# Kernel tuning notes

Measured on AMD Instinct MI355X. Metric: run time of the kernel, lower is better.

Reference implementation:

```python
import jax, jax.numpy as jnp
import numpy as np
from jax.ops import segment_sum

N_NODES = 50000
N_EDGES = 800000
D_IN, D_HID, D_OUT = 128, 128, 64


def setup_inputs() -> dict:
    key = jax.random.key(0)
    ks = jax.random.split(key, 7)
    return {
        "src": jax.random.randint(ks[0], (N_EDGES,), 0, N_NODES, dtype=jnp.int32),
        "dst": jax.random.randint(ks[1], (N_EDGES,), 0, N_NODES, dtype=jnp.int32),
        "x": jax.random.normal(ks[2], (N_NODES, D_IN), dtype=jnp.float32),
        "W1": jax.random.normal(ks[3], (D_IN, D_HID), dtype=jnp.float32) * (1.0 / np.sqrt(D_IN)),
        "b1": jnp.zeros((D_HID,), dtype=jnp.float32),
        "W2": jax.random.normal(ks[4], (D_HID, D_OUT), dtype=jnp.float32) * (1.0 / np.sqrt(D_HID)),
        "b2": jnp.zeros((D_OUT,), dtype=jnp.float32),
    }


def _gcn_layer(src, dst, x, W, b, inv_sqrt_out, inv_sqrt_in):
    # DGL GraphConv, norm='both': h = D_in^{-1/2} A D_out^{-1/2} (x W) + b
    h = (x * inv_sqrt_out[:, None]) @ W          # transform first (in >= out)
    msg = h[src]                                  # gather source messages [E, d]
    agg = segment_sum(msg, dst, num_segments=x.shape[0])
    return agg * inv_sqrt_in[:, None] + b


def reference(src, dst, x, W1, b1, W2, b2):
    n = x.shape[0]
    ones = jnp.ones((src.shape[0],), dtype=x.dtype)
    deg_out = jnp.clip(segment_sum(ones, src, num_segments=n), 1.0)
    deg_in = jnp.clip(segment_sum(ones, dst, num_segments=n), 1.0)
    inv_sqrt_out = jax.lax.rsqrt(deg_out)
    inv_sqrt_in = jax.lax.rsqrt(deg_in)
    h = _gcn_layer(src, dst, x, W1, b1, inv_sqrt_out, inv_sqrt_in)
    h = jax.nn.relu(h)
    h = _gcn_layer(src, dst, h, W2, b2, inv_sqrt_out, inv_sqrt_in)
    return h
```

## Files before the change

kernel.cpp:

```cpp
#include <hip/hip_runtime.h>
#include <hip/hip_fp16.h>

#define D_IN  128
#define D_HID 128
#define D_OUT 64
#define NBMAX 512
#define CHUNK 2048
#define BM 128
#define BK 32
#define FCACHE 3072

__global__ void k_zero(int* __restrict__ cntD, int* __restrict__ cntS, int NB) {
    const int t = threadIdx.x;
    if (t < NB) { cntD[t] = 0; cntS[t] = 0; }
}

__launch_bounds__(256)
__global__ void k_bucket(const int* __restrict__ src, const int* __restrict__ dst,
                         int E, int NB, int cap,
                         int* __restrict__ cntD, int* __restrict__ cntS,
                         unsigned int* __restrict__ storeD, unsigned char* __restrict__ storeS) {
    __shared__ int lcD[NBMAX], lcS[NBMAX];
    __shared__ int lbD[NBMAX], lbS[NBMAX];
    const int t = threadIdx.x;
    const int e0 = blockIdx.x * CHUNK;
    const int e1 = min(e0 + CHUNK, E);

    for (int i = t; i < NB; i += 256) { lcD[i] = 0; lcS[i] = 0; }
    __syncthreads();
    for (int i = e0 + t; i < e1; i += 256) {
        atomicAdd(&lcD[dst[i] >> 7], 1);
        atomicAdd(&lcS[src[i] >> 7], 1);
    }
    __syncthreads();
    for (int i = t; i < NB; i += 256) {
        lbD[i] = lcD[i] ? atomicAdd(&cntD[i], lcD[i]) : 0;
        lbS[i] = lcS[i] ? atomicAdd(&cntS[i], lcS[i]) : 0;
        lcD[i] = 0; lcS[i] = 0;
    }
    __syncthreads();
    for (int i = e0 + t; i < e1; i += 256) {
        const int s = src[i], d = dst[i];
        const int bd = d >> 7;
        const int pd = lbD[bd] + atomicAdd(&lcD[bd], 1);
        storeD[(long long)bd * cap + pd] = (unsigned int)s | ((unsigned int)(d & 127) << 16);
        const int bs = s >> 7;
        const int ps = lbS[bs] + atomicAdd(&lcS[bs], 1);
        storeS[(long long)bs * cap + ps] = (unsigned char)(s & 127);
    }
}

__launch_bounds__(256)
__global__ void k_fin(const unsigned int* __restrict__ storeD, const unsigned char* __restrict__ storeS,
                      const int* __restrict__ cntD, const int* __restrict__ cntS,
                      int cap, int N, int NB, int E,
                      int* __restrict__ rowptr, float* __restrict__ inv_in,
                      float* __restrict__ inv_out, unsigned short* __restrict__ csr_src) {
    __shared__ int fh[128];
    __shared__ int sc[128];
    __shared__ int cur[128];
    __shared__ int red[256];
    __shared__ unsigned int ecache[FCACHE];
    const int b = blockIdx.x, t = threadIdx.x;
    const long long sb = (long long)b * cap;

    int partial = 0;
    for (int i = t; i < b; i += 256) partial += cntD[i];
    red[t] = partial;
    __syncthreads();
    for (int off = 128; off > 0; off >>= 1) {
        if (t < off) red[t] += red[t + off];
        __syncthreads();
    }
    const int base = red[0];

    const int cnt = cntD[b];
    const bool cached = (cnt <= FCACHE);
    if (cached) {
        for (int i = t; i < cnt; i += 256) ecache[i] = storeD[sb + i];
    }

    if (t < 128) fh[t] = 0;
    __syncthreads();
    for (int i = t; i < cnt; i += 256) {
        const unsigned int e = cached ? ecache[i] : storeD[sb + i];
        atomicAdd(&fh[e >> 16], 1);
    }
    __syncthreads();
    if (t < 128) sc[t] = fh[t];
    __syncthreads();
    int inc = (t < 128) ? sc[t] : 0;
    for (int off = 1; off < 128; off <<= 1) {
        int o = (t >= off && t < 128) ? sc[t - off] : 0;
        __syncthreads();
        if (t < 128) { inc += o; sc[t] = inc; }
        __syncthreads();
    }
    if (t < 128) {
        const int excl = inc - fh[t];
        cur[t] = excl;
        const int node = (b << 7) + t;
        if (node < N) {
            rowptr[node] = base + excl;
            inv_in[node] = rsqrtf((float)max(fh[t], 1));
        }
    }
    if (b == NB - 1 && t == 128) rowptr[N] = E;
    __syncthreads();
    for (int i = t; i < cnt; i += 256) {
        const unsigned int e = cached ? ecache[i] : storeD[sb + i];
        const int pos = atomicAdd(&cur[e >> 16], 1);
        csr_src[base + pos] = (unsigned short)(e & 0xFFFFu);
    }

    __syncthreads();
    if (t < 128) fh[t] = 0;
    __syncthreads();
    const int cnts = cntS[b];
    for (int i = t; i < cnts; i += 256) atomicAdd(&fh[storeS[sb + i]], 1);
    __syncthreads();
    if (t < 128) {
        const int node = (b << 7) + t;
        if (node < N) inv_out[node] = rsqrtf((float)max(fh[t], 1));
    }
}

template<int LDN>
__launch_bounds__(256)
__global__ void k_gemm3(const float* __restrict__ X, const float* __restrict__ W,
                        const float* __restrict__ scale, __half* __restrict__ Y, int N) {
    __shared__ float As[BK][BM + 4];
    __shared__ float Bs[BK][64];

    const int t  = threadIdx.x;
    const int tx = t & 15;
    const int ty = t >> 4;
    const int row0 = blockIdx.x * BM;
    const int col0 = blockIdx.y * 64;

    const int xr = t >> 3;
    const int xc = (t & 7) * 4;

    float acc[8][4];
#pragma unroll
    for (int m = 0; m < 8; ++m)
#pragma unroll
        for (int n = 0; n < 4; ++n) acc[m][n] = 0.0f;

    for (int kk = 0; kk < D_IN; kk += BK) {
        __syncthreads();
#pragma unroll
        for (int p = 0; p < 4; ++p) {
            const int r  = p * 32 + xr;
            const int gr = row0 + r;
            float4 v = make_float4(0.f, 0.f, 0.f, 0.f);
            if (gr < N) {
                v = *(const float4*)(X + (long long)gr * D_IN + kk + xc);
                if (scale) { const float s = scale[gr]; v.x *= s; v.y *= s; v.z *= s; v.w *= s; }
            }
            As[xc + 0][r] = v.x;
            As[xc + 1][r] = v.y;
            As[xc + 2][r] = v.z;
            As[xc + 3][r] = v.w;
        }
#pragma unroll
        for (int p = 0; p < 2; ++p) {
            const int flat = p * 256 + t;
            const int kr = flat >> 4;
            const int jc = (flat & 15) * 4;
            *(float4*)&Bs[kr][jc] = *(const float4*)(W + (long long)(kk + kr) * LDN + col0 + jc);
        }
        __syncthreads();

#pragma unroll
        for (int k = 0; k < BK; ++k) {
            const float4 a0 = *(const float4*)&As[k][ty * 8];
            const float4 a1 = *(const float4*)&As[k][ty * 8 + 4];
            const float4 b0 = *(const float4*)&Bs[k][tx * 4];
            const float am[8] = {a0.x, a0.y, a0.z, a0.w, a1.x, a1.y, a1.z, a1.w};
            const float bn[4] = {b0.x, b0.y, b0.z, b0.w};
#pragma unroll
            for (int m = 0; m < 8; ++m)
#pragma unroll
                for (int n = 0; n < 4; ++n)
                    acc[m][n] += am[m] * bn[n];
        }
    }

#pragma unroll
    for (int m = 0; m < 8; ++m) {
        const int gr = row0 + ty * 8 + m;
        if (gr < N) {
            __half2 h0 = __float22half2_rn(make_float2(acc[m][0], acc[m][1]));
            __half2 h1 = __float22half2_rn(make_float2(acc[m][2], acc[m][3]));
            uint2 pk;
            pk.x = *(unsigned int*)&h0;
            pk.y = *(unsigned int*)&h1;
            *(uint2*)(Y + (long long)gr * LDN + col0 + tx * 4) = pk;
        }
    }
}

template<int D, bool RELU>
__launch_bounds__(256)
__global__ void k_gather(const int* __restrict__ rowptr, const unsigned short* __restrict__ csr_src,
                         const __half* __restrict__ Y, const float* __restrict__ inv_in,
                         const float* __restrict__ inv_out, const float* __restrict__ b,
                         float* __restrict__ out, int N) {
    const int wid  = (int)((blockIdx.x * 256u + threadIdx.x) >> 6);
    const int lane = threadIdx.x & 63;
    if (wid >= N) return;

    const int start = rowptr[wid];
    const int end   = rowptr[wid + 1];

    constexpr int LPE = D / 8;
    constexpr int EPW = 64 / LPE;
    const int grp  = lane / LPE;
    const int colh = (lane % LPE) * 8;

    float a[8];
#pragma unroll
    for (int u = 0; u < 8; ++u) a[u] = 0.0f;

    auto accum = [&](uint4 raw) {
        const __half2* h = (const __half2*)&raw;
#pragma unroll
        for (int u = 0; u < 4; ++u) {
            const float2 f = __half22float2(h[u]);
            a[2 * u]     += f.x;
            a[2 * u + 1] += f.y;
        }
    };

    for (int k = start; k < end; k += 64) {
        const int idx = k + lane;
        const int sv  = (idx < end) ? (int)csr_src[idx] : 0;
        const int cnt = min(64, end - k);
        int j = 0;
        for (; j + 4 * EPW <= cnt; j += 4 * EPW) {
            const int s0 = __shfl(sv, j + grp);
            const int s1 = __shfl(sv, j + EPW + grp);
            const int s2 = __shfl(sv, j + 2 * EPW + grp);
            const int s3 = __shfl(sv, j + 3 * EPW + grp);
            const uint4 r0 = *(const uint4*)(Y + (long long)s0 * D + colh);
            const uint4 r1 = *(const uint4*)(Y + (long long)s1 * D + colh);
            const uint4 r2 = *(const uint4*)(Y + (long long)s2 * D + colh);
            const uint4 r3 = *(const uint4*)(Y + (long long)s3 * D + colh);
            accum(r0); accum(r1); accum(r2); accum(r3);
        }
        for (; j < cnt; j += EPW) {
            const int jj = j + grp;
            const int s  = __shfl(sv, jj);
            if (jj < cnt) {
                const uint4 r = *(const uint4*)(Y + (long long)s * D + colh);
                accum(r);
            }
        }
    }

#pragma unroll
    for (int u = 0; u < 8; ++u) a[u] += __shfl_down(a[u], 32);
#pragma unroll
    for (int u = 0; u < 8; ++u) a[u] += __shfl_down(a[u], 16);
    if (EPW == 8) {
#pragma unroll
        for (int u = 0; u < 8; ++u) a[u] += __shfl_down(a[u], 8);
    }

    if (lane < LPE) {
        const float ii = inv_in[wid];
        const float io = RELU ? inv_out[wid] : 0.0f;
        const float4 b0 = *(const float4*)(b + colh);
        const float4 b1 = *(const float4*)(b + colh + 4);
        float r[8];
        r[0] = a[0] * ii + b0.x; r[1] = a[1] * ii + b0.y;
        r[2] = a[2] * ii + b0.z; r[3] = a[3] * ii + b0.w;
        r[4] = a[4] * ii + b1.x; r[5] = a[5] * ii + b1.y;
        r[6] = a[6] * ii + b1.z; r[7] = a[7] * ii + b1.w;
        if (RELU) {
#pragma unroll
            for (int u = 0; u < 8; ++u) r[u] = fmaxf(r[u], 0.0f) * io;
        }
        float* o = out + (long long)wid * D + colh;
        *(float4*)(o)     = make_float4(r[0], r[1], r[2], r[3]);
        *(float4*)(o + 4) = make_float4(r[4], r[5], r[6], r[7]);
    }
}

extern "C" void kernel_launch(void* const* d_in, const int* in_sizes, int n_in,
                              void* d_out, int out_size, void* d_ws, size_t ws_size,
                              hipStream_t stream) {
    const int*   src = (const int*)d_in[0];
    const int*   dst = (const int*)d_in[1];
    const float* x   = (const float*)d_in[2];
    const float* W1  = (const float*)d_in[3];
    const float* b1  = (const float*)d_in[4];
    const float* W2  = (const float*)d_in[5];
    const float* b2  = (const float*)d_in[6];
    float* out = (float*)d_out;

    const int E  = in_sizes[0];
    const int N  = in_sizes[2] / D_IN;
    const int NB = (N + 127) >> 7;
    const int mean = E / NB;
    const int cap  = mean + mean / 4 + 128;

    char* ws = (char*)d_ws;
    size_t off = 0;
    auto alloc = [&](size_t bytes) -> void* {
        void* p = ws + off;
        off += (bytes + 255) & ~(size_t)255;
        return p;
    };
    float*          inv_out = (float*)alloc((size_t)N * 4);
    float*          inv_in  = (float*)alloc((size_t)N * 4);
    int*            rowptr  = (int*)alloc((size_t)(N + 1) * 4);
    int*            cntD    = (int*)alloc((size_t)NB * 4);
    int*            cntS    = (int*)alloc((size_t)NB * 4);
    unsigned int*   storeD  = (unsigned int*)alloc((size_t)NB * cap * 4);
    unsigned char*  storeS  = (unsigned char*)alloc((size_t)NB * cap);
    unsigned short* csr_src = (unsigned short*)alloc((size_t)E * 2);
    __half*         Y1      = (__half*)alloc((size_t)N * D_HID * 2);
    float*          H       = (float*)alloc((size_t)N * D_HID * 4);
    __half*         Y2      = (__half*)alloc((size_t)N * D_OUT * 2);
    (void)ws_size; (void)n_in; (void)out_size;

    k_zero<<<1, 512, 0, stream>>>(cntD, cntS, NB);
    k_bucket<<<(E + CHUNK - 1) / CHUNK, 256, 0, stream>>>(src, dst, E, NB, cap, cntD, cntS, storeD, storeS);
    k_fin<<<NB, 256, 0, stream>>>(storeD, storeS, cntD, cntS, cap, N, NB, E,
                                  rowptr, inv_in, inv_out, csr_src);

    {
        dim3 g((N + BM - 1) / BM, D_HID / 64);
        k_gemm3<D_HID><<<g, 256, 0, stream>>>(x, W1, inv_out, Y1, N);
    }
    k_gather<D_HID, true><<<(N + 3) / 4, 256, 0, stream>>>(rowptr, csr_src, Y1, inv_in, inv_out, b1, H, N);

    {
        dim3 g((N + BM - 1) / BM, D_OUT / 64);
        k_gemm3<D_OUT><<<g, 256, 0, stream>>>(H, W2, nullptr, Y2, N);
    }
    k_gather<D_OUT, false><<<(N + 3) / 4, 256, 0, stream>>>(rowptr, csr_src, Y2, inv_in, nullptr, b2, out, N);
}
```

Before: 144.0 us.

## Use split-bf16 MFMA GEMMs and store hidden activations in fp16

Replaces the FP32 SIMT tiled GEMM with a matrix-core kernel. Each FP32 operand is split into high and low bf16 parts, and three MFMA products approximate FP32 accuracy. The hidden activation H written by the first gather is now fp16 instead of fp32, which halves its write and read traffic. This costs extra conversion work when staging into LDS, a smaller 32-row tile with W reloaded per block, and some precision loss in H.

```diff
diff --git a/kernel.cpp b/kernel.cpp
--- a/kernel.cpp
+++ b/kernel.cpp
@@ -6,9 +6,15 @@
 #define D_OUT 64
 #define NBMAX 512
 #define CHUNK 2048
-#define BM 128
-#define BK 32
 #define FCACHE 3072
+
+typedef __attribute__((ext_vector_type(8))) short bf16x8;
+typedef __attribute__((ext_vector_type(4))) float f32x4;
+
+__device__ __forceinline__ unsigned short f2bf_rne(float f) {
+    unsigned int u = __float_as_uint(f);
+    return (unsigned short)((u + 0x7FFFu + ((u >> 16) & 1u)) >> 16);
+}
 
 __global__ void k_zero(int* __restrict__ cntD, int* __restrict__ cntS, int NB) {
     const int t = threadIdx.x;
@@ -125,88 +131,132 @@
     }
 }
 
-template<int LDN>
+template<int LDN, typename TA>
 __launch_bounds__(256)
-__global__ void k_gemm3(const float* __restrict__ X, const float* __restrict__ W,
-                        const float* __restrict__ scale, __half* __restrict__ Y, int N) {
-    __shared__ float As[BK][BM + 4];
-    __shared__ float Bs[BK][64];
-
-    const int t  = threadIdx.x;
-    const int tx = t & 15;
-    const int ty = t >> 4;
-    const int row0 = blockIdx.x * BM;
+__global__ void k_gemm_mfma(const TA* __restrict__ X, const float* __restrict__ W,
+                            const float* __restrict__ scale, __half* __restrict__ Y, int N) {
+    __shared__ short Ah[32][136], Al[32][136];
+    __shared__ short Bh[64][136], Bl[64][136];
+
+    const int t = threadIdx.x;
+    const int row0 = blockIdx.x * 32;
     const int col0 = blockIdx.y * 64;
 
-    const int xr = t >> 3;
-    const int xc = (t & 7) * 4;
-
-    float acc[8][4];
-#pragma unroll
-    for (int m = 0; m < 8; ++m)
-#pragma unroll
-        for (int n = 0; n < 4; ++n) acc[m][n] = 0.0f;
-
-    for (int kk = 0; kk < D_IN; kk += BK) {
-        __syncthreads();
+    if constexpr (sizeof(TA) == 4) {
 #pragma unroll
         for (int p = 0; p < 4; ++p) {
-            const int r  = p * 32 + xr;
-            const int gr = row0 + r;
+            const int idx = p * 256 + t;
+            const int r   = idx >> 5;
+            const int c4  = (idx & 31) << 2;
+            const int gr  = row0 + r;
             float4 v = make_float4(0.f, 0.f, 0.f, 0.f);
             if (gr < N) {
-                v = *(const float4*)(X + (long long)gr * D_IN + kk + xc);
+                v = *(const float4*)((const float*)X + (long long)gr * 128 + c4);
                 if (scale) { const float s = scale[gr]; v.x *= s; v.y *= s; v.z *= s; v.w *= s; }
             }
-            As[xc + 0][r] = v.x;
-            As[xc + 1][r] = v.y;
-            As[xc + 2][r] = v.z;
-            As[xc + 3][r] = v.w;
-        }
+            const float f[4] = {v.x, v.y, v.z, v.w};
+            short4 h, l;
+            short hh[4], ll[4];
+#pragma unroll
+            for (int i = 0; i < 4; ++i) {
+                const unsigned short hb = f2bf_rne(f[i]);
+                const float hf = __uint_as_float(((unsigned int)hb) << 16);
+                hh[i] = (short)hb;
+                ll[i] = (short)f2bf_rne(f[i] - hf);
+            }
+            h = make_short4(hh[0], hh[1], hh[2], hh[3]);
+            l = make_short4(ll[0], ll[1], ll[2], ll[3]);
+            *(short4*)&Ah[r][c4] = h;
+            *(short4*)&Al[r][c4] = l;
+        }
+    } else {
 #pragma unroll
         for (int p = 0; p < 2; ++p) {
-            const int flat = p * 256 + t;
-            const int kr = flat >> 4;
-            const int jc = (flat & 15) * 4;
-            *(float4*)&Bs[kr][jc] = *(const float4*)(W + (long long)(kk + kr) * LDN + col0 + jc);
-        }
-        __syncthreads();
-
-#pragma unroll
-        for (int k = 0; k < BK; ++k) {
-            const float4 a0 = *(const float4*)&As[k][ty * 8];
-            const float4 a1 = *(const float4*)&As[k][ty * 8 + 4];
-            const float4 b0 = *(const float4*)&Bs[k][tx * 4];
-            const float am[8] = {a0.x, a0.y, a0.z, a0.w, a1.x, a1.y, a1.z, a1.w};
-            const float bn[4] = {b0.x, b0.y, b0.z, b0.w};
-#pragma unroll
-            for (int m = 0; m < 8; ++m)
-#pragma unroll
-                for (int n = 0; n < 4; ++n)
-                    acc[m][n] += am[m] * bn[n];
-        }
-    }
-
-#pragma unroll
-    for (int m = 0; m < 8; ++m) {
-        const int gr = row0 + ty * 8 + m;
-        if (gr < N) {
-            __half2 h0 = __float22half2_rn(make_float2(acc[m][0], acc[m][1]));
-            __half2 h1 = __float22half2_rn(make_float2(acc[m][2], acc[m][3]));
-            uint2 pk;
-            pk.x = *(unsigned int*)&h0;
-            pk.y = *(unsigned int*)&h1;
-            *(uint2*)(Y + (long long)gr * LDN + col0 + tx * 4) = pk;
-        }
-    }
-}
-
-template<int D, bool RELU>
+            const int idx = p * 256 + t;
+            const int r   = idx >> 4;
+            const int c8  = (idx & 15) << 3;
+            const int gr  = row0 + r;
+            uint4 raw = make_uint4(0u, 0u, 0u, 0u);
+            if (gr < N) raw = *(const uint4*)((const __half*)X + (long long)gr * 128 + c8);
+            const __half2* hp = (const __half2*)&raw;
+            short hh[8], ll[8];
+#pragma unroll
+            for (int u = 0; u < 4; ++u) {
+                const float2 f2 = __half22float2(hp[u]);
+                const float f[2] = {f2.x, f2.y};
+#pragma unroll
+                for (int q = 0; q < 2; ++q) {
+                    const unsigned short hb = f2bf_rne(f[q]);
+                    const float hf = __uint_as_float(((unsigned int)hb) << 16);
+                    hh[2 * u + q] = (short)hb;
+                    ll[2 * u + q] = (short)f2bf_rne(f[q] - hf);
+                }
+            }
+            *(short4*)&Ah[r][c8]     = make_short4(hh[0], hh[1], hh[2], hh[3]);
+            *(short4*)&Ah[r][c8 + 4] = make_short4(hh[4], hh[5], hh[6], hh[7]);
+            *(short4*)&Al[r][c8]     = make_short4(ll[0], ll[1], ll[2], ll[3]);
+            *(short4*)&Al[r][c8 + 4] = make_short4(ll[4], ll[5], ll[6], ll[7]);
+        }
+    }
+
+#pragma unroll
+    for (int p = 0; p < 8; ++p) {
+        const int idx = p * 256 + t;
+        const int k   = idx >> 4;
+        const int c4  = (idx & 15) << 2;
+        const float4 v = *(const float4*)(W + (long long)k * LDN + col0 + c4);
+        const float f[4] = {v.x, v.y, v.z, v.w};
+#pragma unroll
+        for (int i = 0; i < 4; ++i) {
+            const unsigned short hb = f2bf_rne(f[i]);
+            const float hf = __uint_as_float(((unsigned int)hb) << 16);
+            Bh[c4 + i][k] = (short)hb;
+            Bl[c4 + i][k] = (short)f2bf_rne(f[i] - hf);
+        }
+    }
+    __syncthreads();
+
+    const int w    = t >> 6;
+    const int lane = t & 63;
+    const int wr = w >> 1, wc = w & 1;
+    const int lrow = lane & 15;
+    const int lk   = (lane >> 4) << 3;
+
+    f32x4 acc0 = {0.f, 0.f, 0.f, 0.f};
+    f32x4 acc1 = {0.f, 0.f, 0.f, 0.f};
+#pragma unroll
+    for (int ks = 0; ks < 4; ++ks) {
+        const int k = ks * 32 + lk;
+        const bf16x8 ah  = *(const bf16x8*)&Ah[wr * 16 + lrow][k];
+        const bf16x8 al  = *(const bf16x8*)&Al[wr * 16 + lrow][k];
+        const bf16x8 bh0 = *(const bf16x8*)&Bh[wc * 32 + lrow][k];
+        const bf16x8 bl0 = *(const bf16x8*)&Bl[wc * 32 + lrow][k];
+        const bf16x8 bh1 = *(const bf16x8*)&Bh[wc * 32 + 16 + lrow][k];
+        const bf16x8 bl1 = *(const bf16x8*)&Bl[wc * 32 + 16 + lrow][k];
+        acc0 = __builtin_amdgcn_mfma_f32_16x16x32_bf16(ah, bh0, acc0, 0, 0, 0);
+        acc0 = __builtin_amdgcn_mfma_f32_16x16x32_bf16(ah, bl0, acc0, 0, 0, 0);
+        acc0 = __builtin_amdgcn_mfma_f32_16x16x32_bf16(al, bh0, acc0, 0, 0, 0);
+        acc1 = __builtin_amdgcn_mfma_f32_16x16x32_bf16(ah, bh1, acc1, 0, 0, 0);
+        acc1 = __builtin_amdgcn_mfma_f32_16x16x32_bf16(ah, bl1, acc1, 0, 0, 0);
+        acc1 = __builtin_amdgcn_mfma_f32_16x16x32_bf16(al, bh1, acc1, 0, 0, 0);
+    }
+
+#pragma unroll
+    for (int i = 0; i < 4; ++i) {
+        const int r = row0 + wr * 16 + ((lane >> 4) << 2) + i;
+        if (r < N) {
+            Y[(long long)r * LDN + col0 + wc * 32 + lrow]      = __float2half(acc0[i]);
+            Y[(long long)r * LDN + col0 + wc * 32 + 16 + lrow] = __float2half(acc1[i]);
+        }
+    }
+}
+
+template<int D, bool RELU, typename TO>
 __launch_bounds__(256)
 __global__ void k_gather(const int* __restrict__ rowptr, const unsigned short* __restrict__ csr_src,
                          const __half* __restrict__ Y, const float* __restrict__ inv_in,
                          const float* __restrict__ inv_out, const float* __restrict__ b,
-                         float* __restrict__ out, int N) {
+                         TO* __restrict__ out, int N) {
     const int wid  = (int)((blockIdx.x * 256u + threadIdx.x) >> 6);
     const int lane = threadIdx.x & 63;
     if (wid >= N) return;
@@ -282,9 +332,20 @@
 #pragma unroll
             for (int u = 0; u < 8; ++u) r[u] = fmaxf(r[u], 0.0f) * io;
         }
-        float* o = out + (long long)wid * D + colh;
-        *(float4*)(o)     = make_float4(r[0], r[1], r[2], r[3]);
-        *(float4*)(o + 4) = make_float4(r[4], r[5], r[6], r[7]);
+        if constexpr (sizeof(TO) == 2) {
+            __half2 h0 = __float22half2_rn(make_float2(r[0], r[1]));
+            __half2 h1 = __float22half2_rn(make_float2(r[2], r[3]));
+            __half2 h2 = __float22half2_rn(make_float2(r[4], r[5]));
+            __half2 h3 = __float22half2_rn(make_float2(r[6], r[7]));
+            uint4 pk;
+            pk.x = *(unsigned int*)&h0; pk.y = *(unsigned int*)&h1;
+            pk.z = *(unsigned int*)&h2; pk.w = *(unsigned int*)&h3;
+            *(uint4*)((__half*)out + (long long)wid * D + colh) = pk;
+        } else {
+            float* o = (float*)out + (long long)wid * D + colh;
+            *(float4*)(o)     = make_float4(r[0], r[1], r[2], r[3]);
+            *(float4*)(o + 4) = make_float4(r[4], r[5], r[6], r[7]);
+        }
     }
 }
 
@@ -322,7 +383,7 @@
     unsigned char*  storeS  = (unsigned char*)alloc((size_t)NB * cap);
     unsigned short* csr_src = (unsigned short*)alloc((size_t)E * 2);
     __half*         Y1      = (__half*)alloc((size_t)N * D_HID * 2);
-    float*          H       = (float*)alloc((size_t)N * D_HID * 4);
+    __half*         H       = (__half*)alloc((size_t)N * D_HID * 2);
     __half*         Y2      = (__half*)alloc((size_t)N * D_OUT * 2);
     (void)ws_size; (void)n_in; (void)out_size;
 
@@ -332,14 +393,14 @@
                                   rowptr, inv_in, inv_out, csr_src);
 
     {
-        dim3 g((N + BM - 1) / BM, D_HID / 64);
-        k_gemm3<D_HID><<<g, 256, 0, stream>>>(x, W1, inv_out, Y1, N);
-    }
-    k_gather<D_HID, true><<<(N + 3) / 4, 256, 0, stream>>>(rowptr, csr_src, Y1, inv_in, inv_out, b1, H, N);
+        dim3 g((N + 31) / 32, D_HID / 64);
+        k_gemm_mfma<D_HID, float><<<g, 256, 0, stream>>>(x, W1, inv_out, Y1, N);
+    }
+    k_gather<D_HID, true, __half><<<(N + 3) / 4, 256, 0, stream>>>(rowptr, csr_src, Y1, inv_in, inv_out, b1, H, N);
 
     {
-        dim3 g((N + BM - 1) / BM, D_OUT / 64);
-        k_gemm3<D_OUT><<<g, 256, 0, stream>>>(H, W2, nullptr, Y2, N);
-    }
-    k_gather<D_OUT, false><<<(N + 3) / 4, 256, 0, stream>>>(rowptr, csr_src, Y2, inv_in, nullptr, b2, out, N);
-}
+        dim3 g((N + 31) / 32, D_OUT / 64);
+        k_gemm_mfma<D_OUT, __half><<<g, 256, 0, stream>>>(H, W2, nullptr, Y2, N);
+    }
+    k_gather<D_OUT, false, float><<<(N + 3) / 4, 256, 0, stream>>>(rowptr, csr_src, Y2, inv_in, nullptr, b2, out, N);
+}
```

New measurement: 144.9 us. No clear change (+0.6%).
